# Kernel optimization log

Measured on AMD Instinct MI355X. Metric: run time of the kernel, lower is better.

## Reference

```python
import jax, jax.numpy as jnp
import numpy as np

N_LAYERS = 8
LAYER_NAMES = ['self', 'cross'] * 4
D_MODEL = 256
NHEAD = 8
HEAD_DIM = D_MODEL // NHEAD
EPS_ATTN = 1e-6
EPS_LN = 1e-5


def _xavier(key, shape):
    fan_in, fan_out = shape[-2], shape[-1]
    limit = float(np.sqrt(6.0 / (fan_in + fan_out)))
    return jax.random.uniform(key, shape, jnp.float32, -limit, limit)


def setup_inputs() -> dict:
    key = jax.random.key(0)
    ks = jax.random.split(key, 9)
    B, L, C = 4, 4800, D_MODEL
    inp = {
        'feat0': jax.random.normal(ks[0], (B, L, C), jnp.float32),
        'feat1': jax.random.normal(ks[1], (B, L, C), jnp.float32),
        # stacked per-layer params (layers are deepcopies, independently init'd)
        'Wq': _xavier(ks[2], (N_LAYERS, C, C)),
        'Wk': _xavier(ks[3], (N_LAYERS, C, C)),
        'Wv': _xavier(ks[4], (N_LAYERS, C, C)),
        'Wm': _xavier(ks[5], (N_LAYERS, C, C)),
        'W1': _xavier(ks[6], (N_LAYERS, 2 * C, 2 * C)),
        'W2': _xavier(ks[7], (N_LAYERS, 2 * C, C)),
        'ln1_w': jnp.ones((N_LAYERS, C), jnp.float32),
        'ln1_b': jnp.zeros((N_LAYERS, C), jnp.float32),
        'ln2_w': jnp.ones((N_LAYERS, C), jnp.float32),
        'ln2_b': jnp.zeros((N_LAYERS, C), jnp.float32),
    }
    return inp


def _layernorm(x, w, b):
    mu = jnp.mean(x, axis=-1, keepdims=True)
    var = jnp.mean(jnp.square(x - mu), axis=-1, keepdims=True)
    return (x - mu) * jax.lax.rsqrt(var + EPS_LN) * w + b


def _encoder_layer(x, source, Wq, Wk, Wv, Wm, W1, W2, ln1_w, ln1_b, ln2_w, ln2_b):
    bs, L, C = x.shape
    S = source.shape[1]
    q = (x @ Wq).reshape(bs, L, NHEAD, HEAD_DIM)
    k = (source @ Wk).reshape(bs, S, NHEAD, HEAD_DIM)
    v = (source @ Wv).reshape(bs, S, NHEAD, HEAD_DIM)
    # linear (kernelized) attention: phi(x) = elu(x) + 1
    Q = jax.nn.elu(q) + 1.0
    K = jax.nn.elu(k) + 1.0
    v_len = S
    v_scaled = v / v_len
    KV = jnp.einsum('nshd,nshv->nhdv', K, v_scaled)          # [N,H,D,D]
    Z = 1.0 / (jnp.einsum('nlhd,nhd->nlh', Q, K.sum(axis=1)) + EPS_ATTN)
    msg = jnp.einsum('nlhd,nhdv,nlh->nlhv', Q, KV, Z) * v_len  # [N,L,H,D]
    msg = msg.reshape(bs, L, C) @ Wm
    msg = _layernorm(msg, ln1_w, ln1_b)
    h = jnp.concatenate([x, msg], axis=-1)                   # [N,L,2C]
    h = jnp.maximum(h @ W1, 0.0) @ W2
    h = _layernorm(h, ln2_w, ln2_b)
    return x + h


def reference(feat0, feat1, Wq, Wk, Wv, Wm, W1, W2, ln1_w, ln1_b, ln2_w, ln2_b):
    for i, name in enumerate(LAYER_NAMES):
        p = (Wq[i], Wk[i], Wv[i], Wm[i], W1[i], W2[i],
             ln1_w[i], ln1_b[i], ln2_w[i], ln2_b[i])
        if name == 'self':
            feat0 = _encoder_layer(feat0, feat0, *p)
            feat1 = _encoder_layer(feat1, feat1, *p)
        else:  # cross
            feat0 = _encoder_layer(feat0, feat1, *p)
            feat1 = _encoder_layer(feat1, feat0, *p)
    return (feat0, feat1)
```

## Files before the change

### kernel.cpp

```cpp
#include <hip/hip_runtime.h>

typedef __attribute__((ext_vector_type(8))) short short8;
typedef __attribute__((ext_vector_type(4))) float f32x4;

#define DEV static __device__ __forceinline__

DEV unsigned short f2bf(float x) {
  union { float f; unsigned int u; } c; c.f = x;
  unsigned int r = c.u + 0x7fffu + ((c.u >> 16) & 1u);
  return (unsigned short)(r >> 16);
}
DEV float bf2f(unsigned short s) {
  union { unsigned int u; float f; } c; c.u = ((unsigned int)s) << 16;
  return c.f;
}
DEV float elu1(float x) { return x > 0.f ? x + 1.f : __expf(x); }

DEV void gload_lds16(const void* g, void* l) {
  __builtin_amdgcn_global_load_lds(
      (const __attribute__((address_space(1))) unsigned int*)g,
      (__attribute__((address_space(3))) unsigned int*)l, 16, 0, 0);
}

__global__ __launch_bounds__(256)
void wprep(const float* __restrict__ src, unsigned short* __restrict__ dst,
           int K, int N, int dls) {
  const int layer = blockIdx.z;
  src += (size_t)layer * K * N;
  dst += (size_t)layer * dls;
  __shared__ float tile[64][65];
  const int n0 = blockIdx.x * 64, k0 = blockIdx.y * 64;
  const int c = threadIdx.x & 63, r4 = threadIdx.x >> 6;
#pragma unroll
  for (int i = 0; i < 16; ++i) {
    int r = (i << 2) + r4;
    tile[r][c] = src[(size_t)(k0 + r) * N + n0 + c];
  }
  __syncthreads();
#pragma unroll
  for (int i = 0; i < 16; ++i) {
    int r = (i << 2) + r4;
    dst[(size_t)(n0 + r) * K + k0 + c] = f2bf(tile[c][r]);
  }
}

__global__ __launch_bounds__(256)
void init_feat(const float* __restrict__ src, float* __restrict__ dstf,
               unsigned short* __restrict__ dstb, int n4) {
  int i = blockIdx.x * 256 + threadIdx.x;
  if (i >= n4) return;
  float4 v = ((const float4*)src)[i];
  ((float4*)dstf)[i] = v;
  ushort4 o;
  o.x = f2bf(v.x); o.y = f2bf(v.y); o.z = f2bf(v.z); o.w = f2bf(v.w);
  ((ushort4*)dstb)[i] = o;
}

template<int EPI>
__global__ __launch_bounds__(256)
void gemm_bt(const unsigned short* __restrict__ A0,
             const unsigned short* __restrict__ A1,
             const unsigned short* __restrict__ BT,
             unsigned short* __restrict__ Cb, unsigned short* __restrict__ Cb2,
             int M, int N, int K, int lda) {
  __shared__ __align__(16) unsigned short As[128 * 64];
  __shared__ __align__(16) unsigned short Bs[128 * 64];
  const int tid = threadIdx.x;
  const int lane = tid & 63, wave = tid >> 6;
  const int tn = N >> 7;
  const int bm = (int)blockIdx.x / tn, bn = (int)blockIdx.x % tn;
  const int wm = (wave >> 1) << 6, wn = (wave & 1) << 6;
  const int lr = lane & 15, lk = lane >> 4;

  f32x4 acc[4][4];
#pragma unroll
  for (int i = 0; i < 4; ++i)
#pragma unroll
    for (int j = 0; j < 4; ++j) acc[i][j] = (f32x4){0.f, 0.f, 0.f, 0.f};

  for (int k0 = 0; k0 < K; k0 += 64) {
#pragma unroll
    for (int i = 0; i < 4; ++i) {
      const int cb = (i << 2) + wave;
      const int id = (cb << 6) + lane;
      const int row = id >> 3, ck = id & 7;
      const int gk = k0 + ((ck ^ (row & 7)) << 3);
      const unsigned short* srcA;
      if (A1) {
        srcA = (gk < 256) ? (A0 + (size_t)(bm * 128 + row) * 256 + gk)
                          : (A1 + (size_t)(bm * 128 + row) * 256 + (gk - 256));
      } else {
        srcA = A0 + (size_t)(bm * 128 + row) * lda + gk;
      }
      gload_lds16(srcA, As + (size_t)cb * 512);
      const unsigned short* srcB = BT + (size_t)(bn * 128 + row) * K + gk;
      gload_lds16(srcB, Bs + (size_t)cb * 512);
    }
    __syncthreads();
#pragma unroll
    for (int kk = 0; kk < 2; ++kk) {
      short8 af[4], bfr[4];
#pragma unroll
      for (int mi = 0; mi < 4; ++mi) {
        const int row = wm + mi * 16 + lr;
        const int ck = ((kk << 2) + lk) ^ (row & 7);
        af[mi] = *(const short8*)(As + row * 64 + ck * 8);
      }
#pragma unroll
      for (int ni = 0; ni < 4; ++ni) {
        const int row = wn + ni * 16 + lr;
        const int ck = ((kk << 2) + lk) ^ (row & 7);
        bfr[ni] = *(const short8*)(Bs + row * 64 + ck * 8);
      }
#pragma unroll
      for (int mi = 0; mi < 4; ++mi)
#pragma unroll
        for (int ni = 0; ni < 4; ++ni)
          acc[mi][ni] = __builtin_amdgcn_mfma_f32_16x16x32_bf16(af[mi], bfr[ni], acc[mi][ni], 0, 0, 0);
    }
    __syncthreads();
  }

  const int cr = lk << 2;
#pragma unroll
  for (int mi = 0; mi < 4; ++mi) {
#pragma unroll
    for (int ni = 0; ni < 4; ++ni) {
      const int colbase = bn * 128 + wn + ni * 16;
#pragma unroll
      for (int j = 0; j < 4; ++j) {
        const int row = bm * 128 + wm + mi * 16 + cr + j;
        const int col = colbase + lr;
        float v = acc[mi][ni][j];
        if (EPI == 1) {
          Cb[(size_t)row * N + col] = f2bf(fmaxf(v, 0.f));
        } else if (EPI == 2) {
          Cb[(size_t)row * N + col] = f2bf(colbase < 256 ? elu1(v) : v);
        } else if (EPI == 3) {
          Cb[(size_t)row * 256 + col] = f2bf(elu1(v));
        } else {
          if (colbase < 256) Cb[(size_t)row * 256 + col] = f2bf(elu1(v));
          else Cb2[(size_t)row * 512 + (col - 256)] = f2bf(colbase < 512 ? elu1(v) : v);
        }
      }
    }
  }
}

template<int EPI>
__global__ __launch_bounds__(512)
void gemm_ln(const unsigned short* __restrict__ A, const unsigned short* __restrict__ BT,
             const float* __restrict__ lnw, const float* __restrict__ lnb,
             const float* __restrict__ xres, float* __restrict__ outf,
             unsigned short* __restrict__ outb, int K) {
  __shared__ __align__(16) unsigned short As[128 * 64];
  __shared__ __align__(16) unsigned short Bs[256 * 64];
  const int tid = threadIdx.x;
  const int lane = tid & 63, wid = tid >> 6;
  const int bm = blockIdx.x;
  const int wm = (wid >> 2) << 6, wn = (wid & 3) << 6;
  const int lr = lane & 15, lk = lane >> 4;

  f32x4 acc[4][4];
#pragma unroll
  for (int i = 0; i < 4; ++i)
#pragma unroll
    for (int j = 0; j < 4; ++j) acc[i][j] = (f32x4){0.f, 0.f, 0.f, 0.f};

  for (int k0 = 0; k0 < K; k0 += 64) {
#pragma unroll
    for (int i = 0; i < 2; ++i) {
      const int cb = i * 8 + wid;
      const int id = (cb << 6) + lane;
      const int row = id >> 3, ck = id & 7;
      const int gk = k0 + ((ck ^ (row & 7)) << 3);
      gload_lds16(A + (size_t)(bm * 128 + row) * K + gk, As + (size_t)cb * 512);
    }
#pragma unroll
    for (int i = 0; i < 4; ++i) {
      const int cb = i * 8 + wid;
      const int id = (cb << 6) + lane;
      const int row = id >> 3, ck = id & 7;
      const int gk = k0 + ((ck ^ (row & 7)) << 3);
      gload_lds16(BT + (size_t)row * K + gk, Bs + (size_t)cb * 512);
    }
    __syncthreads();
#pragma unroll
    for (int kk = 0; kk < 2; ++kk) {
      short8 af[4], bfr[4];
#pragma unroll
      for (int mi = 0; mi < 4; ++mi) {
        const int row = wm + mi * 16 + lr;
        const int ck = ((kk << 2) + lk) ^ (row & 7);
        af[mi] = *(const short8*)(As + row * 64 + ck * 8);
      }
#pragma unroll
      for (int ni = 0; ni < 4; ++ni) {
        const int row = wn + ni * 16 + lr;
        const int ck = ((kk << 2) + lk) ^ (row & 7);
        bfr[ni] = *(const short8*)(Bs + row * 64 + ck * 8);
      }
#pragma unroll
      for (int mi = 0; mi < 4; ++mi)
#pragma unroll
        for (int ni = 0; ni < 4; ++ni)
          acc[mi][ni] = __builtin_amdgcn_mfma_f32_16x16x32_bf16(af[mi], bfr[ni], acc[mi][ni], 0, 0, 0);
    }
    __syncthreads();
  }

  float* red = (float*)As;
  float wv[4], bv[4];
#pragma unroll
  for (int ni = 0; ni < 4; ++ni) {
    wv[ni] = lnw[wn + ni * 16 + lr];
    bv[ni] = lnb[wn + ni * 16 + lr];
  }
#pragma unroll
  for (int mi = 0; mi < 4; ++mi) {
#pragma unroll
    for (int j = 0; j < 4; ++j) {
      float s = 0.f, q = 0.f;
#pragma unroll
      for (int ni = 0; ni < 4; ++ni) {
        float v = acc[mi][ni][j];
        s += v; q += v * v;
      }
#pragma unroll
      for (int o = 1; o < 16; o <<= 1) {
        s += __shfl_xor(s, o);
        q += __shfl_xor(q, o);
      }
      if (lr == 0) {
        int row = wm + mi * 16 + (lk << 2) + j;
        red[row * 8 + (wid & 3) * 2] = s;
        red[row * 8 + (wid & 3) * 2 + 1] = q;
      }
    }
  }
  __syncthreads();
#pragma unroll
  for (int mi = 0; mi < 4; ++mi) {
#pragma unroll
    for (int j = 0; j < 4; ++j) {
      const int row = wm + mi * 16 + (lk << 2) + j;
      const size_t grow = (size_t)bm * 128 + row;
      float s = red[row * 8] + red[row * 8 + 2] + red[row * 8 + 4] + red[row * 8 + 6];
      float q = red[row * 8 + 1] + red[row * 8 + 3] + red[row * 8 + 5] + red[row * 8 + 7];
      float mu = s * (1.f / 256.f);
      float var = q * (1.f / 256.f) - mu * mu;
      float rstd = rsqrtf(var + 1e-5f);
#pragma unroll
      for (int ni = 0; ni < 4; ++ni) {
        int col = wn + ni * 16 + lr;
        float y = (acc[mi][ni][j] - mu) * rstd * wv[ni] + bv[ni];
        if (EPI == 0) {
          outb[grow * 256 + col] = f2bf(y);
        } else {
          float o = xres[grow * 256 + col] + y;
          outf[grow * 256 + col] = o;
          outb[grow * 256 + col] = f2bf(o);
        }
      }
    }
  }
}

__global__ __launch_bounds__(256)
void kv_partial(const unsigned short* __restrict__ kvb, float* __restrict__ part) {
  const int ch = blockIdx.x, h = blockIdx.y, n = blockIdx.z;
  const int t = threadIdx.x, wave = t >> 6, lane = t & 63;
  __shared__ float kb[4][8][36];
  __shared__ float vb[4][8][36];
  const int dq = lane >> 3, vq = lane & 7;
  float a[4][4];
  float ks[4] = {0.f, 0.f, 0.f, 0.f};
#pragma unroll
  for (int i = 0; i < 4; ++i)
#pragma unroll
    for (int j = 0; j < 4; ++j) a[i][j] = 0.f;

  const int s_base = ch * 480 + wave * 120;
  const int half = lane >> 5, l = lane & 31, r = l >> 2, c8 = l & 3;
  const unsigned short* src = kvb + ((size_t)n * 4800 + s_base + r) * 512 +
                              half * 256 + h * 32 + c8 * 8;
  float* dst = (half ? &vb[wave][r][0] : &kb[wave][r][0]) + c8 * 8;

  for (int it = 0; it < 15; ++it) {
    __syncthreads();
    short8 raw = *(const short8*)(src + (size_t)it * 8 * 512);
#pragma unroll
    for (int e = 0; e < 8; ++e) dst[e] = bf2f((unsigned short)raw[e]);
    __syncthreads();
#pragma unroll
    for (int si = 0; si < 8; ++si) {
      float4 kq = *(const float4*)&kb[wave][si][dq * 4];
      float4 vv = *(const float4*)&vb[wave][si][vq * 4];
      ks[0] += kq.x; ks[1] += kq.y; ks[2] += kq.z; ks[3] += kq.w;
      a[0][0] += kq.x * vv.x; a[0][1] += kq.x * vv.y; a[0][2] += kq.x * vv.z; a[0][3] += kq.x * vv.w;
      a[1][0] += kq.y * vv.x; a[1][1] += kq.y * vv.y; a[1][2] += kq.y * vv.z; a[1][3] += kq.y * vv.w;
      a[2][0] += kq.z * vv.x; a[2][1] += kq.z * vv.y; a[2][2] += kq.z * vv.z; a[2][3] += kq.z * vv.w;
      a[3][0] += kq.w * vv.x; a[3][1] += kq.w * vv.y; a[3][2] += kq.w * vv.z; a[3][3] += kq.w * vv.w;
    }
  }
  float* pb = part + ((size_t)((n * 8 + h) * 40 + ch * 4 + wave)) * 1056;
#pragma unroll
  for (int i = 0; i < 4; ++i) {
#pragma unroll
    for (int j = 0; j < 4; ++j) pb[(dq * 4 + i) * 32 + vq * 4 + j] = a[i][j];
    if (vq == 0) pb[1024 + dq * 4 + i] = ks[i];
  }
}

__global__ __launch_bounds__(256)
void kv_reduce(const float* __restrict__ part, unsigned short* __restrict__ KVb,
               float* __restrict__ Ksum) {
  const int nh = blockIdx.x, t = threadIdx.x;
  const float* pb = part + (size_t)nh * 40 * 1056;
#pragma unroll
  for (int j = 0; j < 4; ++j) {
    int e = t * 4 + j;
    float s = 0.f;
    for (int c = 0; c < 40; ++c) s += pb[c * 1056 + e];
    int dd = e >> 5, vv = e & 31;
    size_t addr = ((size_t)(nh * 2 + (vv >> 4)) * 64 + ((dd >> 3) * 16 + (vv & 15))) * 8 + (dd & 7);
    KVb[addr] = f2bf(s);
  }
  if (t < 32) {
    float s = 0.f;
    for (int c = 0; c < 40; ++c) s += pb[c * 1056 + 1024 + t];
    Ksum[nh * 32 + t] = s;
  }
}

__global__ __launch_bounds__(256)
void msg_kernel(const unsigned short* __restrict__ qb, const unsigned short* __restrict__ KVb,
                const float* __restrict__ Ksum, unsigned short* __restrict__ msg) {
  const int n = blockIdx.y;
  const int wave = threadIdx.x >> 6, lane = threadIdx.x & 63;
  const int lr = lane & 15, lk = lane >> 4;
  const int lrow = blockIdx.x * 64 + wave * 16 + lr;
  const unsigned short* qrow = qb + ((size_t)n * 4800 + lrow) * 256;
  const short8* kvv = (const short8*)KVb;
  for (int h = 0; h < 8; ++h) {
    short8 af = *(const short8*)(qrow + h * 32 + lk * 8);
    const float* ksp = Ksum + (n * 8 + h) * 32 + lk * 8;
    float zp = 0.f;
#pragma unroll
    for (int j = 0; j < 8; ++j) zp += bf2f((unsigned short)af[j]) * ksp[j];
    zp += __shfl_xor(zp, 16);
    zp += __shfl_xor(zp, 32);
    float z = 1.f / (zp + 1e-6f);
    short8 b0 = kvv[((size_t)(n * 8 + h) * 2 + 0) * 64 + lane];
    short8 b1 = kvv[((size_t)(n * 8 + h) * 2 + 1) * 64 + lane];
    f32x4 acc0 = (f32x4){0.f, 0.f, 0.f, 0.f}, acc1 = (f32x4){0.f, 0.f, 0.f, 0.f};
    acc0 = __builtin_amdgcn_mfma_f32_16x16x32_bf16(af, b0, acc0, 0, 0, 0);
    acc1 = __builtin_amdgcn_mfma_f32_16x16x32_bf16(af, b1, acc1, 0, 0, 0);
#pragma unroll
    for (int j = 0; j < 4; ++j) {
      int rr = lk * 4 + j;
      float zj = __shfl(z, rr);
      int row = blockIdx.x * 64 + wave * 16 + rr;
      size_t base = ((size_t)n * 4800 + row) * 256 + h * 32;
      msg[base + lr] = f2bf(acc0[j] * zj);
      msg[base + 16 + lr] = f2bf(acc1[j] * zj);
    }
  }
}

extern "C" void kernel_launch(void* const* d_in, const int* in_sizes, int n_in,
                              void* d_out, int out_size, void* d_ws, size_t ws_size,
                              hipStream_t stream) {
  (void)in_sizes; (void)n_in; (void)out_size; (void)ws_size;
  const float* feat0 = (const float*)d_in[0];
  const float* feat1 = (const float*)d_in[1];
  const float* Wq = (const float*)d_in[2];
  const float* Wk = (const float*)d_in[3];
  const float* Wv = (const float*)d_in[4];
  const float* Wm = (const float*)d_in[5];
  const float* W1 = (const float*)d_in[6];
  const float* W2 = (const float*)d_in[7];
  const float* ln1w = (const float*)d_in[8];
  const float* ln1b = (const float*)d_in[9];
  const float* ln2w = (const float*)d_in[10];
  const float* ln2b = (const float*)d_in[11];

  float* F0 = (float*)d_out;
  float* F1 = F0 + (size_t)4915200;

  size_t off = 0;
  auto alloc = [&](size_t bytes) -> void* {
    void* p = (char*)d_ws + off;
    off += (bytes + 255) & ~(size_t)255;
    return p;
  };
  unsigned short* Fb     = (unsigned short*)alloc((size_t)38400 * 256 * 2);
  unsigned short* qb     = (unsigned short*)alloc((size_t)38400 * 256 * 2);
  unsigned short* kvb    = (unsigned short*)alloc((size_t)38400 * 512 * 2);
  unsigned short* msgb   = (unsigned short*)alloc((size_t)38400 * 256 * 2);
  unsigned short* msglnb = (unsigned short*)alloc((size_t)38400 * 256 * 2);
  float*          part   = (float*)alloc((size_t)64 * 40 * 1056 * 4);
  unsigned short* KVb    = (unsigned short*)alloc((size_t)65536 * 2);
  float*          Ksum   = (float*)alloc((size_t)2048 * 4);
  unsigned short* WqkvT  = (unsigned short*)alloc((size_t)8 * 196608 * 2);
  unsigned short* WmT    = (unsigned short*)alloc((size_t)8 * 65536 * 2);
  unsigned short* W1T    = (unsigned short*)alloc((size_t)8 * 262144 * 2);
  unsigned short* W2T    = (unsigned short*)alloc((size_t)8 * 131072 * 2);
  unsigned short* h1b = kvb;
  unsigned short* F0b = Fb;
  unsigned short* F1b = Fb + (size_t)19200 * 256;

  init_feat<<<4800, 256, 0, stream>>>(feat0, F0, F0b, 1228800);
  init_feat<<<4800, 256, 0, stream>>>(feat1, F1, F1b, 1228800);

  wprep<<<dim3(4, 4, 8), 256, 0, stream>>>(Wq, WqkvT, 256, 256, 196608);
  wprep<<<dim3(4, 4, 8), 256, 0, stream>>>(Wk, WqkvT + 65536, 256, 256, 196608);
  wprep<<<dim3(4, 4, 8), 256, 0, stream>>>(Wv, WqkvT + 131072, 256, 256, 196608);
  wprep<<<dim3(4, 4, 8), 256, 0, stream>>>(Wm, WmT, 256, 256, 65536);
  wprep<<<dim3(8, 8, 8), 256, 0, stream>>>(W1, W1T, 512, 512, 262144);
  wprep<<<dim3(4, 8, 8), 256, 0, stream>>>(W2, W2T, 512, 256, 131072);

  auto enc_self = [&](int i) {
    gemm_bt<4><<<1800, 256, 0, stream>>>(Fb, nullptr, WqkvT + (size_t)i * 196608,
                                         qb, kvb, 38400, 768, 256, 256);
    kv_partial<<<dim3(10, 8, 8), 256, 0, stream>>>(kvb, part);
    kv_reduce<<<64, 256, 0, stream>>>(part, KVb, Ksum);
    msg_kernel<<<dim3(75, 8), 256, 0, stream>>>(qb, KVb, Ksum, msgb);
    gemm_ln<0><<<300, 512, 0, stream>>>(msgb, WmT + (size_t)i * 65536,
                                        ln1w + i * 256, ln1b + i * 256,
                                        nullptr, nullptr, msglnb, 256);
    gemm_bt<1><<<1200, 256, 0, stream>>>(Fb, msglnb, W1T + (size_t)i * 262144,
                                         h1b, nullptr, 38400, 512, 512, 256);
    gemm_ln<1><<<300, 512, 0, stream>>>(h1b, W2T + (size_t)i * 131072,
                                        ln2w + i * 256, ln2b + i * 256,
                                        F0, F0, Fb, 512);
  };

  auto enc_cross = [&](float* X, unsigned short* Xb, unsigned short* Sb, int i) {
    gemm_bt<3><<<300, 256, 0, stream>>>(Xb, nullptr, WqkvT + (size_t)i * 196608,
                                        qb, nullptr, 19200, 256, 256, 256);
    gemm_bt<2><<<600, 256, 0, stream>>>(Sb, nullptr, WqkvT + (size_t)i * 196608 + 65536,
                                        kvb, nullptr, 19200, 512, 256, 256);
    kv_partial<<<dim3(10, 8, 4), 256, 0, stream>>>(kvb, part);
    kv_reduce<<<32, 256, 0, stream>>>(part, KVb, Ksum);
    msg_kernel<<<dim3(75, 4), 256, 0, stream>>>(qb, KVb, Ksum, msgb);
    gemm_ln<0><<<150, 512, 0, stream>>>(msgb, WmT + (size_t)i * 65536,
                                        ln1w + i * 256, ln1b + i * 256,
                                        nullptr, nullptr, msglnb, 256);
    gemm_bt<1><<<600, 256, 0, stream>>>(Xb, msglnb, W1T + (size_t)i * 262144,
                                        h1b, nullptr, 19200, 512, 512, 256);
    gemm_ln<1><<<150, 512, 0, stream>>>(h1b, W2T + (size_t)i * 131072,
                                        ln2w + i * 256, ln2b + i * 256,
                                        X, X, Xb, 512);
  };

  for (int i = 0; i < 8; ++i) {
    if ((i & 1) == 0) {
      enc_self(i);
    } else {
      enc_cross(F0, F0b, F1b, i);
      enc_cross(F1, F1b, F0b, i);
    }
  }
}
```

Measured before the change: 1.627 ms.

## Fuse K/V projection with KV reduction and batch Q projection across streams

A new gemm_kv kernel computes the K and V projections in registers and stores them to LDS. From there it reduces them straight into per-head KV and Ksum with float atomics. This removes the global kvb buffer, kv_partial and kv_reduce, and the partial-sum buffer. The Q projection for both features is now one launch at the start of each layer, and msg_kernel takes a row offset. The cost is extra zeroing and conversion launches, atomic contention, and a large LDS and register footprint per block.

```diff
diff --git a/kernel.cpp b/kernel.cpp
--- a/kernel.cpp
+++ b/kernel.cpp
@@ -56,12 +56,18 @@
   ((ushort4*)dstb)[i] = o;
 }
 
+__global__ __launch_bounds__(256)
+void zero_f4(float* __restrict__ p, int n4) {
+  int i = blockIdx.x * 256 + threadIdx.x;
+  if (i < n4) ((float4*)p)[i] = make_float4(0.f, 0.f, 0.f, 0.f);
+}
+
 template<int EPI>
 __global__ __launch_bounds__(256)
 void gemm_bt(const unsigned short* __restrict__ A0,
              const unsigned short* __restrict__ A1,
              const unsigned short* __restrict__ BT,
-             unsigned short* __restrict__ Cb, unsigned short* __restrict__ Cb2,
+             unsigned short* __restrict__ Cb,
              int M, int N, int K, int lda) {
   __shared__ __align__(16) unsigned short As[128 * 64];
   __shared__ __align__(16) unsigned short Bs[128 * 64];
@@ -134,16 +140,140 @@
         float v = acc[mi][ni][j];
         if (EPI == 1) {
           Cb[(size_t)row * N + col] = f2bf(fmaxf(v, 0.f));
-        } else if (EPI == 2) {
-          Cb[(size_t)row * N + col] = f2bf(colbase < 256 ? elu1(v) : v);
-        } else if (EPI == 3) {
+        } else {
           Cb[(size_t)row * 256 + col] = f2bf(elu1(v));
-        } else {
-          if (colbase < 256) Cb[(size_t)row * 256 + col] = f2bf(elu1(v));
-          else Cb2[(size_t)row * 512 + (col - 256)] = f2bf(colbase < 512 ? elu1(v) : v);
         }
       }
     }
+  }
+}
+
+__global__ __launch_bounds__(512)
+void gemm_kv(const unsigned short* __restrict__ A, const unsigned short* __restrict__ BT,
+             float* __restrict__ KVf, float* __restrict__ Ksumf) {
+  __shared__ __align__(16) unsigned short sh[40960];
+  unsigned short* As = sh;
+  unsigned short* Bs = sh + 128 * 64;
+  const int tid = threadIdx.x, lane = tid & 63, wid = tid >> 6;
+  const int n = blockIdx.y, bm = blockIdx.x;
+  const int wm = (wid >> 2) << 6, wn = (wid & 3) << 7;
+  const int lr = lane & 15, lk = lane >> 4;
+  const int row0 = bm * 128;
+  const int valid = min(128, 4800 - row0);
+  const unsigned short* Ab = A + ((size_t)n * 4800 + row0) * 256;
+
+  f32x4 acc[4][8];
+#pragma unroll
+  for (int i = 0; i < 4; ++i)
+#pragma unroll
+    for (int j = 0; j < 8; ++j) acc[i][j] = (f32x4){0.f, 0.f, 0.f, 0.f};
+
+  for (int k0 = 0; k0 < 256; k0 += 64) {
+#pragma unroll
+    for (int j = 0; j < 2; ++j) {
+      int c = j * 512 + tid;
+      int row = c >> 3, ck = c & 7;
+      int gk = k0 + ((ck ^ (row & 7)) << 3);
+      gload_lds16(Ab + (size_t)row * 256 + gk, As + (size_t)c * 8);
+    }
+#pragma unroll
+    for (int j = 0; j < 8; ++j) {
+      int c = j * 512 + tid;
+      int row = c >> 3, ck = c & 7;
+      int gk = k0 + ((ck ^ (row & 7)) << 3);
+      gload_lds16(BT + (size_t)row * 256 + gk, Bs + (size_t)c * 8);
+    }
+    __syncthreads();
+#pragma unroll
+    for (int kk = 0; kk < 2; ++kk) {
+      short8 af[4], bfr[8];
+#pragma unroll
+      for (int mi = 0; mi < 4; ++mi) {
+        int row = wm + mi * 16 + lr;
+        int ck = ((kk << 2) + lk) ^ (row & 7);
+        af[mi] = *(const short8*)(As + row * 64 + ck * 8);
+      }
+#pragma unroll
+      for (int ni = 0; ni < 8; ++ni) {
+        int row = wn + ni * 16 + lr;
+        int ck = ((kk << 2) + lk) ^ (row & 7);
+        bfr[ni] = *(const short8*)(Bs + row * 64 + ck * 8);
+      }
+#pragma unroll
+      for (int mi = 0; mi < 4; ++mi)
+#pragma unroll
+        for (int ni = 0; ni < 8; ++ni)
+          acc[mi][ni] = __builtin_amdgcn_mfma_f32_16x16x32_bf16(af[mi], bfr[ni], acc[mi][ni], 0, 0, 0);
+    }
+    __syncthreads();
+  }
+
+  const int cr = lk << 2;
+  const int dq = lane >> 3, vq = lane & 7;
+  float a[4][4], ks[4] = {0.f, 0.f, 0.f, 0.f};
+#pragma unroll
+  for (int i = 0; i < 4; ++i)
+#pragma unroll
+    for (int j = 0; j < 4; ++j) a[i][j] = 0.f;
+
+#pragma unroll
+  for (int th = 0; th < 2; ++th) {
+    if ((wm >> 6) == th) {
+#pragma unroll
+      for (int mi = 0; mi < 4; ++mi)
+#pragma unroll
+        for (int j = 0; j < 4; ++j) {
+          int r = mi * 16 + cr + j;
+          bool dead = (th * 64 + r) >= valid;
+#pragma unroll
+          for (int ni = 0; ni < 8; ++ni) {
+            int col = wn + ni * 16 + lr;
+            float v = acc[mi][ni][j];
+            sh[r * 512 + col] = dead ? (unsigned short)0
+                                     : f2bf(col < 256 ? elu1(v) : v);
+          }
+        }
+    }
+    __syncthreads();
+    const unsigned short* kbase = sh + wid * 32 + dq * 4;
+    const unsigned short* vbase = sh + 256 + wid * 32 + vq * 4;
+    for (int s = 0; s < 64; ++s) {
+      float kr[4], vr[4];
+#pragma unroll
+      for (int e = 0; e < 4; ++e) kr[e] = bf2f(kbase[s * 512 + e]);
+#pragma unroll
+      for (int e = 0; e < 4; ++e) vr[e] = bf2f(vbase[s * 512 + e]);
+      ks[0] += kr[0]; ks[1] += kr[1]; ks[2] += kr[2]; ks[3] += kr[3];
+#pragma unroll
+      for (int i = 0; i < 4; ++i)
+#pragma unroll
+        for (int j = 0; j < 4; ++j) a[i][j] += kr[i] * vr[j];
+    }
+    __syncthreads();
+  }
+
+  float* kvd = KVf + (size_t)(n * 8 + wid) * 1024;
+  float* ksd = Ksumf + (size_t)(n * 8 + wid) * 32;
+#pragma unroll
+  for (int i = 0; i < 4; ++i) {
+#pragma unroll
+    for (int j = 0; j < 4; ++j)
+      atomicAdd(&kvd[(dq * 4 + i) * 32 + vq * 4 + j], a[i][j]);
+    if (vq == 0) atomicAdd(&ksd[dq * 4 + i], ks[i]);
+  }
+}
+
+__global__ __launch_bounds__(256)
+void kv_cvt(const float* __restrict__ KVf, unsigned short* __restrict__ KVb) {
+  const int nh = blockIdx.x, t = threadIdx.x;
+  const float* src = KVf + (size_t)nh * 1024;
+#pragma unroll
+  for (int j = 0; j < 4; ++j) {
+    int e = t * 4 + j;
+    float s = src[e];
+    int dd = e >> 5, vv = e & 31;
+    size_t addr = ((size_t)(nh * 2 + (vv >> 4)) * 64 + ((dd >> 3) * 16 + (vv & 15))) * 8 + (dd & 7);
+    KVb[addr] = f2bf(s);
   }
 }
 
@@ -267,80 +397,13 @@
 }
 
 __global__ __launch_bounds__(256)
-void kv_partial(const unsigned short* __restrict__ kvb, float* __restrict__ part) {
-  const int ch = blockIdx.x, h = blockIdx.y, n = blockIdx.z;
-  const int t = threadIdx.x, wave = t >> 6, lane = t & 63;
-  __shared__ float kb[4][8][36];
-  __shared__ float vb[4][8][36];
-  const int dq = lane >> 3, vq = lane & 7;
-  float a[4][4];
-  float ks[4] = {0.f, 0.f, 0.f, 0.f};
-#pragma unroll
-  for (int i = 0; i < 4; ++i)
-#pragma unroll
-    for (int j = 0; j < 4; ++j) a[i][j] = 0.f;
-
-  const int s_base = ch * 480 + wave * 120;
-  const int half = lane >> 5, l = lane & 31, r = l >> 2, c8 = l & 3;
-  const unsigned short* src = kvb + ((size_t)n * 4800 + s_base + r) * 512 +
-                              half * 256 + h * 32 + c8 * 8;
-  float* dst = (half ? &vb[wave][r][0] : &kb[wave][r][0]) + c8 * 8;
-
-  for (int it = 0; it < 15; ++it) {
-    __syncthreads();
-    short8 raw = *(const short8*)(src + (size_t)it * 8 * 512);
-#pragma unroll
-    for (int e = 0; e < 8; ++e) dst[e] = bf2f((unsigned short)raw[e]);
-    __syncthreads();
-#pragma unroll
-    for (int si = 0; si < 8; ++si) {
-      float4 kq = *(const float4*)&kb[wave][si][dq * 4];
-      float4 vv = *(const float4*)&vb[wave][si][vq * 4];
-      ks[0] += kq.x; ks[1] += kq.y; ks[2] += kq.z; ks[3] += kq.w;
-      a[0][0] += kq.x * vv.x; a[0][1] += kq.x * vv.y; a[0][2] += kq.x * vv.z; a[0][3] += kq.x * vv.w;
-      a[1][0] += kq.y * vv.x; a[1][1] += kq.y * vv.y; a[1][2] += kq.y * vv.z; a[1][3] += kq.y * vv.w;
-      a[2][0] += kq.z * vv.x; a[2][1] += kq.z * vv.y; a[2][2] += kq.z * vv.z; a[2][3] += kq.z * vv.w;
-      a[3][0] += kq.w * vv.x; a[3][1] += kq.w * vv.y; a[3][2] += kq.w * vv.z; a[3][3] += kq.w * vv.w;
-    }
-  }
-  float* pb = part + ((size_t)((n * 8 + h) * 40 + ch * 4 + wave)) * 1056;
-#pragma unroll
-  for (int i = 0; i < 4; ++i) {
-#pragma unroll
-    for (int j = 0; j < 4; ++j) pb[(dq * 4 + i) * 32 + vq * 4 + j] = a[i][j];
-    if (vq == 0) pb[1024 + dq * 4 + i] = ks[i];
-  }
-}
-
-__global__ __launch_bounds__(256)
-void kv_reduce(const float* __restrict__ part, unsigned short* __restrict__ KVb,
-               float* __restrict__ Ksum) {
-  const int nh = blockIdx.x, t = threadIdx.x;
-  const float* pb = part + (size_t)nh * 40 * 1056;
-#pragma unroll
-  for (int j = 0; j < 4; ++j) {
-    int e = t * 4 + j;
-    float s = 0.f;
-    for (int c = 0; c < 40; ++c) s += pb[c * 1056 + e];
-    int dd = e >> 5, vv = e & 31;
-    size_t addr = ((size_t)(nh * 2 + (vv >> 4)) * 64 + ((dd >> 3) * 16 + (vv & 15))) * 8 + (dd & 7);
-    KVb[addr] = f2bf(s);
-  }
-  if (t < 32) {
-    float s = 0.f;
-    for (int c = 0; c < 40; ++c) s += pb[c * 1056 + 1024 + t];
-    Ksum[nh * 32 + t] = s;
-  }
-}
-
-__global__ __launch_bounds__(256)
 void msg_kernel(const unsigned short* __restrict__ qb, const unsigned short* __restrict__ KVb,
-                const float* __restrict__ Ksum, unsigned short* __restrict__ msg) {
+                const float* __restrict__ Ksum, unsigned short* __restrict__ msg, int qoff) {
   const int n = blockIdx.y;
   const int wave = threadIdx.x >> 6, lane = threadIdx.x & 63;
   const int lr = lane & 15, lk = lane >> 4;
   const int lrow = blockIdx.x * 64 + wave * 16 + lr;
-  const unsigned short* qrow = qb + ((size_t)n * 4800 + lrow) * 256;
+  const unsigned short* qrow = qb + ((size_t)qoff + (size_t)n * 4800 + lrow) * 256;
   const short8* kvv = (const short8*)KVb;
   for (int h = 0; h < 8; ++h) {
     short8 af = *(const short8*)(qrow + h * 32 + lk * 8);
@@ -396,17 +459,16 @@
   };
   unsigned short* Fb     = (unsigned short*)alloc((size_t)38400 * 256 * 2);
   unsigned short* qb     = (unsigned short*)alloc((size_t)38400 * 256 * 2);
-  unsigned short* kvb    = (unsigned short*)alloc((size_t)38400 * 512 * 2);
+  unsigned short* h1b    = (unsigned short*)alloc((size_t)38400 * 512 * 2);
   unsigned short* msgb   = (unsigned short*)alloc((size_t)38400 * 256 * 2);
   unsigned short* msglnb = (unsigned short*)alloc((size_t)38400 * 256 * 2);
-  float*          part   = (float*)alloc((size_t)64 * 40 * 1056 * 4);
+  float*          attn   = (float*)alloc((size_t)67584 * 4);
   unsigned short* KVb    = (unsigned short*)alloc((size_t)65536 * 2);
-  float*          Ksum   = (float*)alloc((size_t)2048 * 4);
   unsigned short* WqkvT  = (unsigned short*)alloc((size_t)8 * 196608 * 2);
   unsigned short* WmT    = (unsigned short*)alloc((size_t)8 * 65536 * 2);
   unsigned short* W1T    = (unsigned short*)alloc((size_t)8 * 262144 * 2);
   unsigned short* W2T    = (unsigned short*)alloc((size_t)8 * 131072 * 2);
-  unsigned short* h1b = kvb;
+  float* Ksumf = attn + 65536;
   unsigned short* F0b = Fb;
   unsigned short* F1b = Fb + (size_t)19200 * 256;
 
@@ -420,46 +482,37 @@
   wprep<<<dim3(8, 8, 8), 256, 0, stream>>>(W1, W1T, 512, 512, 262144);
   wprep<<<dim3(4, 8, 8), 256, 0, stream>>>(W2, W2T, 512, 256, 131072);
 
-  auto enc_self = [&](int i) {
-    gemm_bt<4><<<1800, 256, 0, stream>>>(Fb, nullptr, WqkvT + (size_t)i * 196608,
-                                         qb, kvb, 38400, 768, 256, 256);
-    kv_partial<<<dim3(10, 8, 8), 256, 0, stream>>>(kvb, part);
-    kv_reduce<<<64, 256, 0, stream>>>(part, KVb, Ksum);
-    msg_kernel<<<dim3(75, 8), 256, 0, stream>>>(qb, KVb, Ksum, msgb);
-    gemm_ln<0><<<300, 512, 0, stream>>>(msgb, WmT + (size_t)i * 65536,
-                                        ln1w + i * 256, ln1b + i * 256,
-                                        nullptr, nullptr, msglnb, 256);
-    gemm_bt<1><<<1200, 256, 0, stream>>>(Fb, msglnb, W1T + (size_t)i * 262144,
-                                         h1b, nullptr, 38400, 512, 512, 256);
-    gemm_ln<1><<<300, 512, 0, stream>>>(h1b, W2T + (size_t)i * 131072,
-                                        ln2w + i * 256, ln2b + i * 256,
-                                        F0, F0, Fb, 512);
+  auto attn_block = [&](const unsigned short* src, int nb, int qoff, int i) {
+    zero_f4<<<66, 256, 0, stream>>>(attn, 16896);
+    gemm_kv<<<dim3(38, nb), 512, 0, stream>>>(src, WqkvT + (size_t)i * 196608 + 65536,
+                                              attn, Ksumf);
+    kv_cvt<<<nb * 8, 256, 0, stream>>>(attn, KVb);
+    msg_kernel<<<dim3(75, nb), 256, 0, stream>>>(qb, KVb, Ksumf, msgb, qoff);
   };
 
-  auto enc_cross = [&](float* X, unsigned short* Xb, unsigned short* Sb, int i) {
-    gemm_bt<3><<<300, 256, 0, stream>>>(Xb, nullptr, WqkvT + (size_t)i * 196608,
-                                        qb, nullptr, 19200, 256, 256, 256);
-    gemm_bt<2><<<600, 256, 0, stream>>>(Sb, nullptr, WqkvT + (size_t)i * 196608 + 65536,
-                                        kvb, nullptr, 19200, 512, 256, 256);
-    kv_partial<<<dim3(10, 8, 4), 256, 0, stream>>>(kvb, part);
-    kv_reduce<<<32, 256, 0, stream>>>(part, KVb, Ksum);
-    msg_kernel<<<dim3(75, 4), 256, 0, stream>>>(qb, KVb, Ksum, msgb);
-    gemm_ln<0><<<150, 512, 0, stream>>>(msgb, WmT + (size_t)i * 65536,
-                                        ln1w + i * 256, ln1b + i * 256,
-                                        nullptr, nullptr, msglnb, 256);
-    gemm_bt<1><<<600, 256, 0, stream>>>(Xb, msglnb, W1T + (size_t)i * 262144,
-                                        h1b, nullptr, 19200, 512, 512, 256);
-    gemm_ln<1><<<150, 512, 0, stream>>>(h1b, W2T + (size_t)i * 131072,
-                                        ln2w + i * 256, ln2b + i * 256,
-                                        X, X, Xb, 512);
+  auto ffn = [&](unsigned short* Xb, float* X, int M, int i) {
+    const int g = M >> 7;
+    gemm_ln<0><<<g, 512, 0, stream>>>(msgb, WmT + (size_t)i * 65536,
+                                      ln1w + i * 256, ln1b + i * 256,
+                                      nullptr, nullptr, msglnb, 256);
+    gemm_bt<1><<<g * 4, 256, 0, stream>>>(Xb, msglnb, W1T + (size_t)i * 262144,
+                                          h1b, M, 512, 512, 256);
+    gemm_ln<1><<<g, 512, 0, stream>>>(h1b, W2T + (size_t)i * 131072,
+                                      ln2w + i * 256, ln2b + i * 256,
+                                      X, X, Xb, 512);
   };
 
   for (int i = 0; i < 8; ++i) {
+    gemm_bt<3><<<600, 256, 0, stream>>>(Fb, nullptr, WqkvT + (size_t)i * 196608,
+                                        qb, 38400, 256, 256, 256);
     if ((i & 1) == 0) {
-      enc_self(i);
+      attn_block(Fb, 8, 0, i);
+      ffn(Fb, F0, 38400, i);
     } else {
-      enc_cross(F0, F0b, F1b, i);
-      enc_cross(F1, F1b, F0b, i);
-    }
-  }
-}
+      attn_block(F1b, 4, 0, i);
+      ffn(F0b, F0, 19200, i);
+      attn_block(F0b, 4, 19200, i);
+      ffn(F1b, F1, 19200, i);
+    }
+  }
+}
```

Measured after the change: 1.955 ms. +20.2%, slower.

## Stage GEMM epilogues through LDS, shrink LN tiles, batch cross-layer Q projection

Applied to the files above, without the earlier changes.

The gemm_bt and gemm_ln epilogues now write bf16 results into a padded LDS tile, then store them to global memory as 16-byte row-contiguous chunks instead of scattered 2-byte stores. gemm_ln switches to 64-row tiles with 256 threads, which doubles the block count for better occupancy on the narrow LN GEMMs. In cross layers the Q projection for both features runs in one launch over 38400 rows, and msg_kernel takes a row offset to read the second half. The extra LDS traffic and barriers are the added cost.

```diff
diff --git a/kernel.cpp b/kernel.cpp
--- a/kernel.cpp
+++ b/kernel.cpp
@@ -63,8 +63,9 @@
              const unsigned short* __restrict__ BT,
              unsigned short* __restrict__ Cb, unsigned short* __restrict__ Cb2,
              int M, int N, int K, int lda) {
-  __shared__ __align__(16) unsigned short As[128 * 64];
-  __shared__ __align__(16) unsigned short Bs[128 * 64];
+  __shared__ __align__(16) unsigned short smem[16896];
+  unsigned short* As = smem;
+  unsigned short* Bs = smem + 8192;
   const int tid = threadIdx.x;
   const int lane = tid & 63, wave = tid >> 6;
   const int tn = N >> 7;
@@ -121,44 +122,53 @@
     __syncthreads();
   }
 
+  unsigned short* dst;
+  int cstride, colofs, act;
+  if (EPI == 1)      { dst = Cb;  cstride = N;   colofs = bn * 128; act = 1; }
+  else if (EPI == 2) { dst = Cb;  cstride = 512; colofs = bn * 128; act = (bn < 2) ? 2 : 0; }
+  else if (EPI == 3) { dst = Cb;  cstride = 256; colofs = bn * 128; act = 2; }
+  else {
+    if (bn < 2) { dst = Cb;  cstride = 256; colofs = bn * 128;       act = 2; }
+    else        { dst = Cb2; cstride = 512; colofs = bn * 128 - 256; act = (bn < 4) ? 2 : 0; }
+  }
+
+  unsigned short* Ct = smem;
   const int cr = lk << 2;
 #pragma unroll
-  for (int mi = 0; mi < 4; ++mi) {
-#pragma unroll
-    for (int ni = 0; ni < 4; ++ni) {
-      const int colbase = bn * 128 + wn + ni * 16;
+  for (int mi = 0; mi < 4; ++mi)
+#pragma unroll
+    for (int ni = 0; ni < 4; ++ni)
 #pragma unroll
       for (int j = 0; j < 4; ++j) {
-        const int row = bm * 128 + wm + mi * 16 + cr + j;
-        const int col = colbase + lr;
         float v = acc[mi][ni][j];
-        if (EPI == 1) {
-          Cb[(size_t)row * N + col] = f2bf(fmaxf(v, 0.f));
-        } else if (EPI == 2) {
-          Cb[(size_t)row * N + col] = f2bf(colbase < 256 ? elu1(v) : v);
-        } else if (EPI == 3) {
-          Cb[(size_t)row * 256 + col] = f2bf(elu1(v));
-        } else {
-          if (colbase < 256) Cb[(size_t)row * 256 + col] = f2bf(elu1(v));
-          else Cb2[(size_t)row * 512 + (col - 256)] = f2bf(colbase < 512 ? elu1(v) : v);
-        }
-      }
-    }
+        v = (act == 1) ? fmaxf(v, 0.f) : (act == 2) ? elu1(v) : v;
+        Ct[(wm + mi * 16 + cr + j) * 132 + (wn + ni * 16 + lr)] = f2bf(v);
+      }
+  __syncthreads();
+  const int rr = lane >> 4, cc8 = (lane & 15) << 3;
+#pragma unroll
+  for (int s = 0; s < 8; ++s) {
+    const int rl = (wave << 5) + (s << 2) + rr;
+    uint2 lo = *(const uint2*)(Ct + rl * 132 + cc8);
+    uint2 hi = *(const uint2*)(Ct + rl * 132 + cc8 + 4);
+    uint4 val = make_uint4(lo.x, lo.y, hi.x, hi.y);
+    *(uint4*)(dst + (size_t)(bm * 128 + rl) * cstride + colofs + cc8) = val;
   }
 }
 
 template<int EPI>
-__global__ __launch_bounds__(512)
+__global__ __launch_bounds__(256)
 void gemm_ln(const unsigned short* __restrict__ A, const unsigned short* __restrict__ BT,
              const float* __restrict__ lnw, const float* __restrict__ lnb,
              const float* __restrict__ xres, float* __restrict__ outf,
              unsigned short* __restrict__ outb, int K) {
-  __shared__ __align__(16) unsigned short As[128 * 64];
-  __shared__ __align__(16) unsigned short Bs[256 * 64];
+  __shared__ __align__(16) unsigned short smem[4096 + 16896];
+  unsigned short* As = smem;
+  unsigned short* Bs = smem + 4096;
   const int tid = threadIdx.x;
   const int lane = tid & 63, wid = tid >> 6;
   const int bm = blockIdx.x;
-  const int wm = (wid >> 2) << 6, wn = (wid & 3) << 6;
+  const int wn = wid << 6;
   const int lr = lane & 15, lk = lane >> 4;
 
   f32x4 acc[4][4];
@@ -170,15 +180,15 @@
   for (int k0 = 0; k0 < K; k0 += 64) {
 #pragma unroll
     for (int i = 0; i < 2; ++i) {
-      const int cb = i * 8 + wid;
+      const int cb = (i << 2) + wid;
       const int id = (cb << 6) + lane;
       const int row = id >> 3, ck = id & 7;
       const int gk = k0 + ((ck ^ (row & 7)) << 3);
-      gload_lds16(A + (size_t)(bm * 128 + row) * K + gk, As + (size_t)cb * 512);
-    }
-#pragma unroll
-    for (int i = 0; i < 4; ++i) {
-      const int cb = i * 8 + wid;
+      gload_lds16(A + (size_t)(bm * 64 + row) * K + gk, As + (size_t)cb * 512);
+    }
+#pragma unroll
+    for (int i = 0; i < 8; ++i) {
+      const int cb = (i << 2) + wid;
       const int id = (cb << 6) + lane;
       const int row = id >> 3, ck = id & 7;
       const int gk = k0 + ((ck ^ (row & 7)) << 3);
@@ -190,7 +200,7 @@
       short8 af[4], bfr[4];
 #pragma unroll
       for (int mi = 0; mi < 4; ++mi) {
-        const int row = wm + mi * 16 + lr;
+        const int row = mi * 16 + lr;
         const int ck = ((kk << 2) + lk) ^ (row & 7);
         af[mi] = *(const short8*)(As + row * 64 + ck * 8);
       }
@@ -209,7 +219,8 @@
     __syncthreads();
   }
 
-  float* red = (float*)As;
+  float* red = (float*)smem;
+  const int cr = lk << 2;
   float wv[4], bv[4];
 #pragma unroll
   for (int ni = 0; ni < 4; ++ni) {
@@ -232,19 +243,21 @@
         q += __shfl_xor(q, o);
       }
       if (lr == 0) {
-        int row = wm + mi * 16 + (lk << 2) + j;
-        red[row * 8 + (wid & 3) * 2] = s;
-        red[row * 8 + (wid & 3) * 2 + 1] = q;
+        int row = mi * 16 + cr + j;
+        red[row * 8 + wid * 2] = s;
+        red[row * 8 + wid * 2 + 1] = q;
       }
     }
   }
   __syncthreads();
+
+  unsigned short* Pt = Bs;
 #pragma unroll
   for (int mi = 0; mi < 4; ++mi) {
 #pragma unroll
     for (int j = 0; j < 4; ++j) {
-      const int row = wm + mi * 16 + (lk << 2) + j;
-      const size_t grow = (size_t)bm * 128 + row;
+      const int row = mi * 16 + cr + j;
+      const size_t grow = (size_t)bm * 64 + row;
       float s = red[row * 8] + red[row * 8 + 2] + red[row * 8 + 4] + red[row * 8 + 6];
       float q = red[row * 8 + 1] + red[row * 8 + 3] + red[row * 8 + 5] + red[row * 8 + 7];
       float mu = s * (1.f / 256.f);
@@ -255,15 +268,28 @@
         int col = wn + ni * 16 + lr;
         float y = (acc[mi][ni][j] - mu) * rstd * wv[ni] + bv[ni];
         if (EPI == 0) {
-          outb[grow * 256 + col] = f2bf(y);
+          Pt[row * 264 + col] = f2bf(y);
         } else {
           float o = xres[grow * 256 + col] + y;
           outf[grow * 256 + col] = o;
-          outb[grow * 256 + col] = f2bf(o);
+          Pt[row * 264 + col] = f2bf(o);
         }
       }
     }
   }
+  __syncthreads();
+  const int rr = lane >> 4, cc8 = (lane & 15) << 3;
+#pragma unroll
+  for (int s = 0; s < 4; ++s)
+#pragma unroll
+    for (int ch = 0; ch < 2; ++ch) {
+      const int rl = (wid << 4) + (s << 2) + rr;
+      const int col = (ch << 7) + cc8;
+      uint2 lo = *(const uint2*)(Pt + rl * 264 + col);
+      uint2 hi = *(const uint2*)(Pt + rl * 264 + col + 4);
+      uint4 val = make_uint4(lo.x, lo.y, hi.x, hi.y);
+      *(uint4*)(outb + (size_t)(bm * 64 + rl) * 256 + col) = val;
+    }
 }
 
 __global__ __launch_bounds__(256)
@@ -335,12 +361,12 @@
 
 __global__ __launch_bounds__(256)
 void msg_kernel(const unsigned short* __restrict__ qb, const unsigned short* __restrict__ KVb,
-                const float* __restrict__ Ksum, unsigned short* __restrict__ msg) {
+                const float* __restrict__ Ksum, unsigned short* __restrict__ msg, int qoff) {
   const int n = blockIdx.y;
   const int wave = threadIdx.x >> 6, lane = threadIdx.x & 63;
   const int lr = lane & 15, lk = lane >> 4;
   const int lrow = blockIdx.x * 64 + wave * 16 + lr;
-  const unsigned short* qrow = qb + ((size_t)n * 4800 + lrow) * 256;
+  const unsigned short* qrow = qb + ((size_t)qoff + (size_t)n * 4800 + lrow) * 256;
   const short8* kvv = (const short8*)KVb;
   for (int h = 0; h < 8; ++h) {
     short8 af = *(const short8*)(qrow + h * 32 + lk * 8);
@@ -420,46 +446,41 @@
   wprep<<<dim3(8, 8, 8), 256, 0, stream>>>(W1, W1T, 512, 512, 262144);
   wprep<<<dim3(4, 8, 8), 256, 0, stream>>>(W2, W2T, 512, 256, 131072);
 
-  auto enc_self = [&](int i) {
-    gemm_bt<4><<<1800, 256, 0, stream>>>(Fb, nullptr, WqkvT + (size_t)i * 196608,
-                                         qb, kvb, 38400, 768, 256, 256);
-    kv_partial<<<dim3(10, 8, 8), 256, 0, stream>>>(kvb, part);
-    kv_reduce<<<64, 256, 0, stream>>>(part, KVb, Ksum);
-    msg_kernel<<<dim3(75, 8), 256, 0, stream>>>(qb, KVb, Ksum, msgb);
-    gemm_ln<0><<<300, 512, 0, stream>>>(msgb, WmT + (size_t)i * 65536,
+  auto ffn = [&](unsigned short* Xb, float* X, int M, int i) {
+    const int g64 = M >> 6, g128 = M >> 7;
+    gemm_ln<0><<<g64, 256, 0, stream>>>(msgb, WmT + (size_t)i * 65536,
                                         ln1w + i * 256, ln1b + i * 256,
                                         nullptr, nullptr, msglnb, 256);
-    gemm_bt<1><<<1200, 256, 0, stream>>>(Fb, msglnb, W1T + (size_t)i * 262144,
-                                         h1b, nullptr, 38400, 512, 512, 256);
-    gemm_ln<1><<<300, 512, 0, stream>>>(h1b, W2T + (size_t)i * 131072,
-                                        ln2w + i * 256, ln2b + i * 256,
-                                        F0, F0, Fb, 512);
-  };
-
-  auto enc_cross = [&](float* X, unsigned short* Xb, unsigned short* Sb, int i) {
-    gemm_bt<3><<<300, 256, 0, stream>>>(Xb, nullptr, WqkvT + (size_t)i * 196608,
-                                        qb, nullptr, 19200, 256, 256, 256);
-    gemm_bt<2><<<600, 256, 0, stream>>>(Sb, nullptr, WqkvT + (size_t)i * 196608 + 65536,
-                                        kvb, nullptr, 19200, 512, 256, 256);
-    kv_partial<<<dim3(10, 8, 4), 256, 0, stream>>>(kvb, part);
-    kv_reduce<<<32, 256, 0, stream>>>(part, KVb, Ksum);
-    msg_kernel<<<dim3(75, 4), 256, 0, stream>>>(qb, KVb, Ksum, msgb);
-    gemm_ln<0><<<150, 512, 0, stream>>>(msgb, WmT + (size_t)i * 65536,
-                                        ln1w + i * 256, ln1b + i * 256,
-                                        nullptr, nullptr, msglnb, 256);
-    gemm_bt<1><<<600, 256, 0, stream>>>(Xb, msglnb, W1T + (size_t)i * 262144,
-                                        h1b, nullptr, 19200, 512, 512, 256);
-    gemm_ln<1><<<150, 512, 0, stream>>>(h1b, W2T + (size_t)i * 131072,
+    gemm_bt<1><<<g128 * 4, 256, 0, stream>>>(Xb, msglnb, W1T + (size_t)i * 262144,
+                                             h1b, nullptr, M, 512, 512, 256);
+    gemm_ln<1><<<g64, 256, 0, stream>>>(h1b, W2T + (size_t)i * 131072,
                                         ln2w + i * 256, ln2b + i * 256,
                                         X, X, Xb, 512);
   };
 
   for (int i = 0; i < 8; ++i) {
     if ((i & 1) == 0) {
-      enc_self(i);
+      gemm_bt<4><<<1800, 256, 0, stream>>>(Fb, nullptr, WqkvT + (size_t)i * 196608,
+                                           qb, kvb, 38400, 768, 256, 256);
+      kv_partial<<<dim3(10, 8, 8), 256, 0, stream>>>(kvb, part);
+      kv_reduce<<<64, 256, 0, stream>>>(part, KVb, Ksum);
+      msg_kernel<<<dim3(75, 8), 256, 0, stream>>>(qb, KVb, Ksum, msgb, 0);
+      ffn(Fb, F0, 38400, i);
     } else {
-      enc_cross(F0, F0b, F1b, i);
-      enc_cross(F1, F1b, F0b, i);
-    }
-  }
-}
+      gemm_bt<3><<<600, 256, 0, stream>>>(Fb, nullptr, WqkvT + (size_t)i * 196608,
+                                          qb, nullptr, 38400, 256, 256, 256);
+      gemm_bt<2><<<600, 256, 0, stream>>>(F1b, nullptr, WqkvT + (size_t)i * 196608 + 65536,
+                                          kvb, nullptr, 19200, 512, 256, 256);
+      kv_partial<<<dim3(10, 8, 4), 256, 0, stream>>>(kvb, part);
+      kv_reduce<<<32, 256, 0, stream>>>(part, KVb, Ksum);
+      msg_kernel<<<dim3(75, 4), 256, 0, stream>>>(qb, KVb, Ksum, msgb, 0);
+      ffn(F0b, F0, 19200, i);
+      gemm_bt<2><<<600, 256, 0, stream>>>(F0b, nullptr, WqkvT + (size_t)i * 196608 + 65536,
+                                          kvb, nullptr, 19200, 512, 256, 256);
+      kv_partial<<<dim3(10, 8, 4), 256, 0, stream>>>(kvb, part);
+      kv_reduce<<<32, 256, 0, stream>>>(part, KVb, Ksum);
+      msg_kernel<<<dim3(75, 4), 256, 0, stream>>>(qb, KVb, Ksum, msgb, 19200);
+      ffn(F1b, F1, 19200, i);
+    }
+  }
+}
```

After: 1.633 ms. About the same (+0.4%).
